# Kernel optimization log

Hardware: AMD Instinct MI355X
Metric: run time of the kernel (lower is better)

## Reference

```python
import jax, jax.numpy as jnp
import numpy as np

B, T = 32, 512
D_TOK, D_OH, D_DEP = 256, 32, 32
D = D_TOK + D_OH + D_DEP  # tree_input_size = 320
H = 64                    # tree_lstm_h_size
P, L, ROOT = 16384, 16, 8 # pairs, path length, root position on path
N = P * L
E = P * (L - 1)
NUM_LEVELS = 9            # max level = max(ROOT, L-1-ROOT) = 8 -> levels 0..8


def _structure():
    # Each subgraph is a shortest path in the dependency tree; edges on both
    # sides point toward the topological root (position ROOT).
    pos = np.arange(L)
    par = np.where(pos < ROOT, pos + 1, np.where(pos > ROOT, pos - 1, pos))
    base = (np.arange(P) * L)[:, None]
    parent_of = (base + par[None, :]).reshape(-1).astype(np.int32)
    nodes = (base + pos[None, :]).reshape(-1).astype(np.int32)
    is_root = np.tile(pos == ROOT, P)
    child = nodes[~is_root]
    parent = parent_of[~is_root]
    level_up = np.tile(np.where(pos <= ROOT, pos, L - 1 - pos), P).astype(np.int32)
    level_down = np.tile(np.abs(pos - ROOT), P).astype(np.int32)
    root_idx = (np.arange(P) * L + ROOT).astype(np.int32)
    start_idx = (np.arange(P) * L).astype(np.int32)
    end_idx = (np.arange(P) * L + (L - 1)).astype(np.int32)
    return child, parent, parent_of, level_up, level_down, root_idx, start_idx, end_idx


def setup_inputs() -> dict:
    key = jax.random.key(0)
    ks = jax.random.split(key, 24)
    sc = 0.02
    ch, pa, po, lu, ld, ri, si, ei = _structure()
    inp = {
        'token_embs': jax.random.normal(ks[0], (B, T, D_TOK), jnp.float32),
        'one_hot_embs': (jax.random.uniform(ks[1], (B, T, D_OH)) < 0.1).astype(jnp.float32),
        'dep_embs': jax.random.normal(ks[2], (B, T, D_DEP), jnp.float32),
        'node_b_idx': jax.random.randint(ks[3], (N,), 0, B, jnp.int32),
        'node_t_idx': jax.random.randint(ks[4], (N,), 0, T, jnp.int32),
        'child': jnp.asarray(ch), 'parent': jnp.asarray(pa),
        'parent_of': jnp.asarray(po),
        'level_up': jnp.asarray(lu), 'level_down': jnp.asarray(ld),
        'root_idx': jnp.asarray(ri), 'start_idx': jnp.asarray(si), 'end_idx': jnp.asarray(ei),
        # child-sum Tree-LSTM params, upward (bottom-up) direction
        'W_iou_up': jax.random.normal(ks[5], (D, 3 * H)) * sc,
        'U_iou_up': jax.random.normal(ks[6], (H, 3 * H)) * sc,
        'b_iou_up': jnp.zeros((3 * H,), jnp.float32),
        'W_f_up': jax.random.normal(ks[7], (D, H)) * sc,
        'U_f_up': jax.random.normal(ks[8], (H, H)) * sc,
        'b_f_up': jnp.zeros((H,), jnp.float32),
        # downward (top-down) direction
        'W_iou_dn': jax.random.normal(ks[9], (D, 3 * H)) * sc,
        'U_iou_dn': jax.random.normal(ks[10], (H, 3 * H)) * sc,
        'b_iou_dn': jnp.zeros((3 * H,), jnp.float32),
        'W_f_dn': jax.random.normal(ks[11], (D, H)) * sc,
        'U_f_dn': jax.random.normal(ks[12], (H, H)) * sc,
        'b_f_dn': jnp.zeros((H,), jnp.float32),
    }
    return inp


def _tree_lstm(x, child, parent, level, x_iou, x_f, U_iou, U_f):
    # Level-synchronous child-sum Tree-LSTM toward parents (bottom-up).
    n = x.shape[0]
    h0 = jnp.zeros((n, H), x.dtype)
    c0 = jnp.zeros((n, H), x.dtype)

    def step(carry, t):
        h, c = carry
        hs = jax.ops.segment_sum(h[child], parent, num_segments=n)          # sum child h
        f = jax.nn.sigmoid(x_f[parent] + h[child] @ U_f)                    # per-edge forget
        fc = jax.ops.segment_sum(f * c[child], parent, num_segments=n)
        i, o, u = jnp.split(x_iou + hs @ U_iou, 3, axis=-1)
        c_new = jax.nn.sigmoid(i) * jnp.tanh(u) + fc
        h_new = jax.nn.sigmoid(o) * jnp.tanh(c_new)
        m = (level == t)[:, None]
        return (jnp.where(m, h_new, h), jnp.where(m, c_new, c)), None

    (h, c), _ = jax.lax.scan(step, (h0, c0), jnp.arange(NUM_LEVELS))
    return h


def _tree_lstm_down(x, parent_of, level_down, x_iou, x_f, U_iou, U_f):
    # Top-down pass: each node has exactly one predecessor (its parent).
    n = x.shape[0]
    not_root = (level_down != 0).astype(x.dtype)[:, None]
    h0 = jnp.zeros((n, H), x.dtype)
    c0 = jnp.zeros((n, H), x.dtype)

    def step(carry, t):
        h, c = carry
        hp = h[parent_of] * not_root
        cp = c[parent_of] * not_root
        f = jax.nn.sigmoid(x_f + hp @ U_f)
        i, o, u = jnp.split(x_iou + hp @ U_iou, 3, axis=-1)
        c_new = jax.nn.sigmoid(i) * jnp.tanh(u) + f * cp
        h_new = jax.nn.sigmoid(o) * jnp.tanh(c_new)
        m = (level_down == t)[:, None]
        return (jnp.where(m, h_new, h), jnp.where(m, c_new, c)), None

    (h, c), _ = jax.lax.scan(step, (h0, c0), jnp.arange(NUM_LEVELS))
    return h


def reference(token_embs, one_hot_embs, dep_embs, node_b_idx, node_t_idx,
              child, parent, parent_of, level_up, level_down,
              root_idx, start_idx, end_idx,
              W_iou_up, U_iou_up, b_iou_up, W_f_up, U_f_up, b_f_up,
              W_iou_dn, U_iou_dn, b_iou_dn, W_f_dn, U_f_dn, b_f_dn):
    # node_embs = cat(token, one_hot, dep) gathered at subgraph node ids (_ID)
    full = jnp.concatenate((token_embs, one_hot_embs, dep_embs), axis=-1)  # [B,T,D]
    x = full[node_b_idx, node_t_idx]                                       # [N,D]

    # precompute input projections once
    xi_u = x @ W_iou_up + b_iou_up
    xf_u = x @ W_f_up + b_f_up
    xi_d = x @ W_iou_dn + b_iou_dn
    xf_d = x @ W_f_dn + b_f_dn

    h_up = _tree_lstm(x, child, parent, level_up, xi_u, xf_u, U_iou_up, U_f_up)
    h_dn = _tree_lstm_down(x, parent_of, level_down, xi_d, xf_d, U_iou_dn, U_f_dn)

    # tree_lstm_out.view(-1,2,H): slot 0 = bottom-up, slot 1 = top-down
    tree_pair_embs = jnp.concatenate(
        (h_up[root_idx], h_dn[start_idx], h_dn[end_idx]), axis=-1)          # [P, 3H]
    return tree_pair_embs
```

## Files before the change

kernel.cpp:

```cpp
#include <hip/hip_runtime.h>
#include <hip/hip_fp16.h>


typedef _Float16 f16x8 __attribute__((ext_vector_type(8)));
typedef _Float16 f16x4 __attribute__((ext_vector_type(4)));
typedef _Float16 f16x2 __attribute__((ext_vector_type(2)));
typedef float f32x4 __attribute__((ext_vector_type(4)));

#define NP 16
#define N2K 2.8853900817779268f

__device__ __forceinline__ void async16(const void* g, void* l) {
    __builtin_amdgcn_global_load_lds(
        (const __attribute__((address_space(1))) void*)g,
        (__attribute__((address_space(3))) void*)l, 16, 0, 0);
}
__device__ __forceinline__ void lgkm_barrier() {
    asm volatile("s_waitcnt lgkmcnt(0)\n\ts_barrier" ::: "memory");
}
__device__ __forceinline__ f32x4 exp2v(f32x4 x) {
    f32x4 y;
    y[0] = __builtin_amdgcn_exp2f(x[0]);
    y[1] = __builtin_amdgcn_exp2f(x[1]);
    y[2] = __builtin_amdgcn_exp2f(x[2]);
    y[3] = __builtin_amdgcn_exp2f(x[3]);
    return y;
}
__device__ __forceinline__ f32x4 rcpv(f32x4 x) {
    f32x4 y;
    y[0] = __builtin_amdgcn_rcpf(x[0]);
    y[1] = __builtin_amdgcn_rcpf(x[1]);
    y[2] = __builtin_amdgcn_rcpf(x[2]);
    y[3] = __builtin_amdgcn_rcpf(x[3]);
    return y;
}

__global__ __launch_bounds__(256) void prep_kernel(
    const float* __restrict__ Wi_u, const float* __restrict__ Ui_u,
    const float* __restrict__ bi_u, const float* __restrict__ Wf_u,
    const float* __restrict__ Uf_u, const float* __restrict__ bf_u,
    const float* __restrict__ Wi_d, const float* __restrict__ Ui_d,
    const float* __restrict__ bi_d, const float* __restrict__ Wf_d,
    const float* __restrict__ Uf_d, const float* __restrict__ bf_d,
    _Float16* __restrict__ Bx, _Float16* __restrict__ Upk,
    float* __restrict__ pb)
{
    int idx = blockIdx.x * 256 + threadIdx.x;
    if (idx < 512) {
        int d = idx >> 8, c = idx & 255, u = c >> 2, g = c & 3;
        const float* bio = d ? bi_d : bi_u;
        const float* bf  = d ? bf_d : bf_u;
        float s = (g == 2) ? -N2K : -0.5f * N2K;
        pb[idx] = s * ((g < 3) ? bio[g * 64 + u] : bf[u]);
    }
    if (idx < 163840) {
        int d = idx / 81920, r1 = idx % 81920;
        int c = r1 / 320, k = r1 % 320, u = c >> 2, g = c & 3;
        const float* Wio = d ? Wi_d : Wi_u;
        const float* Wf  = d ? Wf_d : Wf_u;
        float s = (g == 2) ? -N2K : -0.5f * N2K;
        Bx[idx] = (_Float16)(s * ((g < 3) ? Wio[k * 192 + g * 64 + u]
                                          : Wf[k * 64 + u]));
    } else {
        int j = idx - 163840;
        int d = j >> 14, r2 = j & 16383;
        int g = r2 >> 12, u = (r2 >> 6) & 63, k = r2 & 63;
        const float* Uio = d ? Ui_d : Ui_u;
        const float* Uf  = d ? Uf_d : Uf_u;
        float s = (g == 2) ? -N2K : -0.5f * N2K;
        Upk[j] = (_Float16)(s * ((g < 3) ? Uio[k * 192 + g * 64 + u]
                                         : Uf[k * 64 + u]));
    }
}

__global__ __launch_bounds__(256, 2) void xp_gemm(
    const float* __restrict__ tok, const float* __restrict__ oh,
    const float* __restrict__ dep,
    const _Float16* __restrict__ Bx, const float* __restrict__ pb,
    _Float16* __restrict__ XP)
{
    __shared__ _Float16 At[32 * 64];
    __shared__ _Float16 Btl[256 * 64];
    const int dir = blockIdx.x & 1, mt = blockIdx.x >> 1;
    const int tid = threadIdx.x, lane = tid & 63, w = tid >> 6;
    const int l15 = lane & 15, qd = lane >> 4;
    const int rsub = lane >> 3, pg = lane & 7;
    const int kg = (pg - rsub) & 7;
    const int koff = kg * 8;
    const int rowbase = mt * 32;
    const _Float16* Bb = Bx + (size_t)dir * 81920 + (w * 64 + rsub) * 320 + koff;

    f32x4 acc[2][4];
    #pragma unroll
    for (int i = 0; i < 2; ++i)
        #pragma unroll
        for (int j = 0; j < 4; ++j) acc[i][j] = (f32x4){0.f, 0.f, 0.f, 0.f};

    #pragma unroll
    for (int kt = 0; kt < 5; ++kt) {
        {
            int row = rowbase + w * 8 + rsub;
            int g = kt * 8 + kg;
            const float* src = (g < 32) ? tok + (size_t)row * 256 + g * 8
                             : (g < 36) ? oh  + (size_t)row * 32 + (g - 32) * 8
                                        : dep + (size_t)row * 32 + (g - 36) * 8;
            float4 f0 = *(const float4*)src;
            float4 f1 = *(const float4*)(src + 4);
            f16x8 v;
            v[0] = (_Float16)f0.x; v[1] = (_Float16)f0.y;
            v[2] = (_Float16)f0.z; v[3] = (_Float16)f0.w;
            v[4] = (_Float16)f1.x; v[5] = (_Float16)f1.y;
            v[6] = (_Float16)f1.z; v[7] = (_Float16)f1.w;
            *(f16x8*)&At[(w * 8 + rsub) * 64 + pg * 8] = v;
        }
        #pragma unroll
        for (int is = 0; is < 8; ++is)
            async16(Bb + (size_t)is * 8 * 320 + kt * 64,
                    &Btl[(w * 64 + is * 8) * 64]);
        __syncthreads();
        #pragma unroll
        for (int s = 0; s < 2; ++s) {
            const int g0 = s * 4 + qd;
            f16x8 af[2];
            #pragma unroll
            for (int i = 0; i < 2; ++i) {
                int R = i * 16 + l15;
                af[i] = *(const f16x8*)&At[R * 64 + ((g0 + R) & 7) * 8];
            }
            #pragma unroll
            for (int j = 0; j < 4; ++j) {
                int C = j * 64 + w * 16 + l15;
                f16x8 bf = *(const f16x8*)&Btl[C * 64 + ((g0 + C) & 7) * 8];
                #pragma unroll
                for (int i = 0; i < 2; ++i)
                    acc[i][j] = __builtin_amdgcn_mfma_f32_16x16x32_f16(
                        af[i], bf, acc[i][j], 0, 0, 0);
            }
        }
        __syncthreads();
    }
    #pragma unroll
    for (int i = 0; i < 2; ++i)
        #pragma unroll
        for (int j = 0; j < 4; ++j) {
            int colp = j * 64 + w * 16 + l15;
            float bias = pb[dir * 256 + colp];
            #pragma unroll
            for (int r = 0; r < 4; ++r) {
                int row = rowbase + i * 16 + qd * 4 + r;
                XP[(size_t)row * 512 + dir * 256 + colp] =
                    (_Float16)(acc[i][j][r] + bias);
            }
        }
}

template<int RPP>
__device__ __forceinline__ void gather_xp(
    const char* __restrict__ XPd, const int (*btl)[NP],
    int p0, int p1, int unit, int qd, f16x4* px)
{
    #pragma unroll
    for (int i = 0; i < RPP; ++i)
        #pragma unroll
        for (int r = 0; r < 4; ++r) {
            int row = i * 16 + qd * 4 + r;
            int pl  = (RPP == 2) ? (row >> 1) : row;
            int pos = (RPP == 2) ? ((row & 1) ? p1 : p0) : p0;
            px[i * 4 + r] = *(const f16x4*)(XPd + btl[pos][pl] + unit * 8);
        }
}

template<int RPP>
__device__ __forceinline__ void side_level(
    const f16x8 (*bfr)[4], const f16x4* px,
    const _Float16 (*hR)[68], const _Float16 (*cR)[68],
    _Float16 (*hW)[68], _Float16 (*cWl)[68],
    f16x2* crR, f16x2* crW, int cregr, int cwEn,
    float* __restrict__ out, int pair0,
    int rs0, int rs1, int oc0, int oc1,
    int unit, int l15, int qd)
{
    f32x4 acc[RPP][4];
    #pragma unroll
    for (int i = 0; i < RPP; ++i)
        #pragma unroll
        for (int r = 0; r < 4; ++r) {
            f16x4 g4 = px[i * 4 + r];
            acc[i][0][r] = (float)g4[0];
            acc[i][1][r] = (float)g4[1];
            acc[i][2][r] = (float)g4[2];
            acc[i][3][r] = (float)g4[3];
        }

    if (rs0 >= 0) {
        __builtin_amdgcn_s_setprio(1);
        #pragma unroll
        for (int s = 0; s < 2; ++s)
            #pragma unroll
            for (int i = 0; i < RPP; ++i) {
                int R = i * 16 + l15;
                int arow = (RPP == 2) ? ((R & ~1) | ((R & 1) ? rs1 : rs0))
                                      : (R * 2 + rs0);
                f16x8 af = *(const f16x8*)&hR[arow][s * 32 + qd * 8];
                #pragma unroll
                for (int g = 0; g < 4; ++g)
                    acc[i][g] = __builtin_amdgcn_mfma_f32_16x16x32_f16(
                        af, bfr[s][g], acc[i][g], 0, 0, 0);
            }
        __builtin_amdgcn_s_setprio(0);
    }

    const int nocin = (rs0 < 0 && rs1 < 0);
    #pragma unroll
    for (int i = 0; i < RPP; ++i) {
        f32x4 EA = exp2v(acc[i][0]);
        f32x4 EO = exp2v(acc[i][1]);
        f32x4 EB = exp2v(acc[i][2]);
        f32x4 PQ = (1.f + EA) * (1.f + EB);
        f32x4 CN;
        if (nocin) {
            CN = (1.f - EB) * rcpv(PQ);
        } else {
            f32x4 CIN;
            #pragma unroll
            for (int r = 0; r < 4; ++r) {
                int row = i * 16 + qd * 4 + r;
                int pl   = (RPP == 2) ? (row >> 1) : row;
                int slot = (RPP == 2) ? (row & 1) : 0;
                int rs = slot ? rs1 : rs0;
                if (RPP == 2 && cregr)
                    CIN[r] = (float)crR[i * 2 + (r >> 1)][rs];
                else
                    CIN[r] = (rs >= 0) ? (float)cR[pl * 2 + rs][unit] : 0.f;
            }
            f32x4 EC = exp2v(acc[i][3]);
            f32x4 PC = 1.f + EC;
            f32x4 NUM = CIN * PQ + (1.f - EB) * PC;
            CN = NUM * rcpv(PQ * PC);
        }
        f32x4 EE = exp2v(-N2K * CN);
        f32x4 H = (1.f - EE) * rcpv((1.f + EE) * (1.f + EO));
        #pragma unroll
        for (int r = 0; r < 4; ++r) {
            int row = i * 16 + qd * 4 + r;
            int pl   = (RPP == 2) ? (row >> 1) : row;
            int slot = (RPP == 2) ? (row & 1) : 0;
            int oc = slot ? oc1 : oc0;
            if (oc >= 0) {
                out[(size_t)(pair0 + pl) * 192 + oc + unit] = H[r];
            } else {
                hW[pl * 2 + slot][unit] = (_Float16)H[r];
                if (cwEn) cWl[pl * 2 + slot][unit] = (_Float16)CN[r];
                if (RPP == 2) crW[i * 2 + (r >> 1)][r & 1] = (_Float16)CN[r];
            }
        }
    }
}

__device__ __forceinline__ void root_level(
    const f16x8 (*bfr)[4], const f16x4* px,
    const _Float16 (*hR0)[68], const _Float16 (*cR0)[68],
    const _Float16 (*hR1)[68], const _Float16 (*cR1)[68],
    float* __restrict__ out, int pair0, int unit, int l15, int qd)
{
    f32x4 aio[3], aF7, aF9;
    #pragma unroll
    for (int r = 0; r < 4; ++r) {
        f16x4 g4 = px[r];
        aio[0][r] = (float)g4[0];
        aio[1][r] = (float)g4[1];
        aio[2][r] = (float)g4[2];
        aF7[r] = (float)g4[3];
        aF9[r] = (float)g4[3];
    }
    __builtin_amdgcn_s_setprio(1);
    #pragma unroll
    for (int s = 0; s < 2; ++s) {
        f16x8 v7 = *(const f16x8*)&hR0[l15 * 2 + 0][s * 32 + qd * 8];
        f16x8 v9 = *(const f16x8*)&hR1[l15 * 2 + 1][s * 32 + qd * 8];
        f16x8 vs = v7 + v9;
        aio[0] = __builtin_amdgcn_mfma_f32_16x16x32_f16(vs, bfr[s][0], aio[0], 0, 0, 0);
        aio[1] = __builtin_amdgcn_mfma_f32_16x16x32_f16(vs, bfr[s][1], aio[1], 0, 0, 0);
        aio[2] = __builtin_amdgcn_mfma_f32_16x16x32_f16(vs, bfr[s][2], aio[2], 0, 0, 0);
        aF7 = __builtin_amdgcn_mfma_f32_16x16x32_f16(v7, bfr[s][3], aF7, 0, 0, 0);
        aF9 = __builtin_amdgcn_mfma_f32_16x16x32_f16(v9, bfr[s][3], aF9, 0, 0, 0);
    }
    __builtin_amdgcn_s_setprio(0);
    f32x4 C7, C9;
    #pragma unroll
    for (int r = 0; r < 4; ++r) {
        int pl = qd * 4 + r;
        C7[r] = (float)cR0[pl * 2 + 0][unit];
        C9[r] = (float)cR1[pl * 2 + 1][unit];
    }
    f32x4 EA = exp2v(aio[0]);
    f32x4 EO = exp2v(aio[1]);
    f32x4 EB = exp2v(aio[2]);
    f32x4 E7 = exp2v(aF7);
    f32x4 E9 = exp2v(aF9);
    f32x4 PQ  = (1.f + EA) * (1.f + EB);
    f32x4 S7  = 1.f + E7, S9 = 1.f + E9;
    f32x4 S79 = S7 * S9;
    f32x4 NUM = PQ * (C7 * S9 + C9 * S7) + (1.f - EB) * S79;
    f32x4 CN  = NUM * rcpv(PQ * S79);
    f32x4 EE  = exp2v(-N2K * CN);
    f32x4 H   = (1.f - EE) * rcpv((1.f + EE) * (1.f + EO));
    #pragma unroll
    for (int r = 0; r < 4; ++r) {
        int pl = qd * 4 + r;
        out[(size_t)(pair0 + pl) * 192 + unit] = H[r];
    }
}

__global__ __launch_bounds__(256, 2) void tree_kernel(
    const int* __restrict__ nb, const int* __restrict__ nt,
    const _Float16* __restrict__ XP, const _Float16* __restrict__ Upk,
    float* __restrict__ out)
{
    __shared__ _Float16 hS[2][2][NP * 2][68];
    __shared__ _Float16 cS[2][2][NP * 2][68];
    __shared__ int btl[16][NP];

    const int tid = threadIdx.x, lane = tid & 63, w = tid >> 6;
    const int l15 = lane & 15, qd = lane >> 4;
    const int unit = w * 16 + l15;
    const int pair0 = blockIdx.x * NP;

    {
        int pos = tid >> 4, pl = tid & 15;
        int node = (pair0 + pl) * 16 + pos;
        btl[pos][pl] = (nb[node] * 512 + nt[node]) * 1024;
    }

    f16x8 bU[2][4], bD[2][4];
    #pragma unroll
    for (int s = 0; s < 2; ++s)
        #pragma unroll
        for (int g = 0; g < 4; ++g) {
            bU[s][g] = *(const f16x8*)(Upk + (g * 64 + unit) * 64 + s * 32 + qd * 8);
            bD[s][g] = *(const f16x8*)(Upk + 16384 + (g * 64 + unit) * 64 + s * 32 + qd * 8);
        }

    __syncthreads();

    const char* XPu = (const char*)XP;
    const char* XPdn = XPu + 512;

    f16x2 creg[2][2][4] = {};

    f16x4 pxu[3][8], pxd[8];
    gather_xp<2>(XPu, btl, 0, 15, unit, qd, pxu[0]);
    gather_xp<2>(XPu, btl, 1, 14, unit, qd, pxu[1]);

    #pragma unroll
    for (int t = 0; t < 9; ++t) {
        const int pt = t & 1, pw = pt ^ 1;
        const int cur = t % 3, nx2 = (t + 2) % 3;
        if (t == 0)      gather_xp<1>(XPdn, btl, 8, 8, unit, qd, pxd);
        else if (t == 8) gather_xp<1>(XPdn, btl, 0, 0, unit, qd, pxd);
        else             gather_xp<2>(XPdn, btl, 8 - t, 8 + t, unit, qd, pxd);
        if (t < 5)       gather_xp<2>(XPu, btl, t + 2, 13 - t, unit, qd, pxu[nx2]);
        else if (t == 5) gather_xp<1>(XPu, btl, 7, 7, unit, qd, pxu[nx2]);
        else if (t == 6) gather_xp<1>(XPu, btl, 8, 8, unit, qd, pxu[nx2]);

        if (t < 7)
            side_level<2>(bU, pxu[cur], hS[pt][0], cS[pt][0],
                          hS[pw][0], cS[pw][0],
                          creg[pt][0], creg[pw][0],
                          (t >= 1) ? 1 : 0, (t == 6) ? 1 : 0,
                          out, pair0,
                          t ? 0 : -1, t ? 1 : -1, -1, -1, unit, l15, qd);
        else if (t == 7)
            side_level<1>(bU, pxu[cur], hS[pt][0], cS[pt][0],
                          hS[pw][0], cS[pw][0],
                          creg[pt][0], creg[pw][0], 0, 1,
                          out, pair0,
                          0, 0, -1, -1, unit, l15, qd);
        else
            root_level(bU, pxu[cur], hS[0][0], cS[0][0], hS[1][0], cS[1][0],
                       out, pair0, unit, l15, qd);

        if (t == 0)
            side_level<1>(bD, pxd, hS[pt][1], cS[pt][1],
                          hS[pw][1], cS[pw][1],
                          creg[pt][1], creg[pw][1], 0, 1,
                          out, pair0,
                          -1, -1, -1, -1, unit, l15, qd);
        else if (t == 8)
            side_level<1>(bD, pxd, hS[pt][1], cS[pt][1],
                          hS[pw][1], cS[pw][1],
                          creg[pt][1], creg[pw][1], 0, 0,
                          out, pair0,
                          0, 0, 64, 64, unit, l15, qd);
        else
            side_level<2>(bD, pxd, hS[pt][1], cS[pt][1],
                          hS[pw][1], cS[pw][1],
                          creg[pt][1], creg[pw][1],
                          (t >= 2) ? 1 : 0, (t == 7) ? 1 : 0,
                          out, pair0,
                          0, (t == 1) ? 0 : 1, -1, (t == 7) ? 128 : -1,
                          unit, l15, qd);

        lgkm_barrier();
    }
}

extern "C" void kernel_launch(void* const* d_in, const int* in_sizes, int n_in,
                              void* d_out, int out_size, void* d_ws, size_t ws_size,
                              hipStream_t stream)
{
    const float* tok  = (const float*)d_in[0];
    const float* ohp  = (const float*)d_in[1];
    const float* dep  = (const float*)d_in[2];
    const int*   nb   = (const int*)d_in[3];
    const int*   nt   = (const int*)d_in[4];
    const float* Wi_u = (const float*)d_in[13];
    const float* Ui_u = (const float*)d_in[14];
    const float* bi_u = (const float*)d_in[15];
    const float* Wf_u = (const float*)d_in[16];
    const float* Uf_u = (const float*)d_in[17];
    const float* bf_u = (const float*)d_in[18];
    const float* Wi_d = (const float*)d_in[19];
    const float* Ui_d = (const float*)d_in[20];
    const float* bi_d = (const float*)d_in[21];
    const float* Wf_d = (const float*)d_in[22];
    const float* Uf_d = (const float*)d_in[23];
    const float* bf_d = (const float*)d_in[24];

    char* ws = (char*)d_ws;
    _Float16* Bx  = (_Float16*)(ws);
    _Float16* Upk = (_Float16*)(ws + 0x50000);
    float*    pb  = (float*)   (ws + 0x60000);
    _Float16* XP  = (_Float16*)(ws + (12u << 20));
    float* out = (float*)d_out;

    prep_kernel<<<768, 256, 0, stream>>>(Wi_u, Ui_u, bi_u, Wf_u, Uf_u, bf_u,
                                         Wi_d, Ui_d, bi_d, Wf_d, Uf_d, bf_d,
                                         Bx, Upk, pb);
    xp_gemm<<<1024, 256, 0, stream>>>(tok, ohp, dep, Bx, pb, XP);
    tree_kernel<<<1024, 256, 0, stream>>>(nb, nt, XP, Upk, out);

    (void)in_sizes; (void)n_in; (void)out_size; (void)ws_size;
}
```

Baseline: 185.5 us.

## Halve pairs per block in tree kernel to raise occupancy

Each tree_kernel block now handles 8 pairs instead of 16, doubling the grid to 2048 blocks and raising launch bounds to 5 blocks per CU. Per-level work shrinks from two 16-row MFMA tiles to one, with rows duplicated or masked in single-sided levels. The upward gather prefetch depth drops from two levels to one, and the s_setprio hints are removed. This cuts register and LDS pressure to hide latency through more resident waves, but loses deeper prefetch and wastes half the MFMA rows on single-position levels.

```diff
diff --git a/kernel.cpp b/kernel.cpp
--- a/kernel.cpp
+++ b/kernel.cpp
@@ -7,7 +7,7 @@
 typedef _Float16 f16x2 __attribute__((ext_vector_type(2)));
 typedef float f32x4 __attribute__((ext_vector_type(4)));
 
-#define NP 16
+#define NP 8
 #define N2K 2.8853900817779268f
 
 __device__ __forceinline__ void async16(const void* g, void* l) {
@@ -154,23 +154,21 @@
         }
 }
 
-template<int RPP>
+template<int TWO>
 __device__ __forceinline__ void gather_xp(
     const char* __restrict__ XPd, const int (*btl)[NP],
     int p0, int p1, int unit, int qd, f16x4* px)
 {
     #pragma unroll
-    for (int i = 0; i < RPP; ++i)
-        #pragma unroll
-        for (int r = 0; r < 4; ++r) {
-            int row = i * 16 + qd * 4 + r;
-            int pl  = (RPP == 2) ? (row >> 1) : row;
-            int pos = (RPP == 2) ? ((row & 1) ? p1 : p0) : p0;
-            px[i * 4 + r] = *(const f16x4*)(XPd + btl[pos][pl] + unit * 8);
-        }
-}
-
-template<int RPP>
+    for (int r = 0; r < 4; ++r) {
+        int row = qd * 4 + r;
+        int pl  = TWO ? (row >> 1) : (row & 7);
+        int pos = TWO ? ((row & 1) ? p1 : p0) : p0;
+        px[r] = *(const f16x4*)(XPd + btl[pos][pl] + unit * 8);
+    }
+}
+
+template<int TWO>
 __device__ __forceinline__ void side_level(
     const f16x8 (*bfr)[4], const f16x4* px,
     const _Float16 (*hR)[68], const _Float16 (*cR)[68],
@@ -180,78 +178,71 @@
     int rs0, int rs1, int oc0, int oc1,
     int unit, int l15, int qd)
 {
-    f32x4 acc[RPP][4];
-    #pragma unroll
-    for (int i = 0; i < RPP; ++i)
+    f32x4 acc[4];
+    #pragma unroll
+    for (int r = 0; r < 4; ++r) {
+        f16x4 g4 = px[r];
+        acc[0][r] = (float)g4[0];
+        acc[1][r] = (float)g4[1];
+        acc[2][r] = (float)g4[2];
+        acc[3][r] = (float)g4[3];
+    }
+
+    if (rs0 >= 0) {
+        #pragma unroll
+        for (int s = 0; s < 2; ++s) {
+            int R = l15;
+            int arow = TWO ? ((R & ~1) | ((R & 1) ? rs1 : rs0))
+                           : ((R & 7) * 2 + rs0);
+            f16x8 af = *(const f16x8*)&hR[arow][s * 32 + qd * 8];
+            #pragma unroll
+            for (int g = 0; g < 4; ++g)
+                acc[g] = __builtin_amdgcn_mfma_f32_16x16x32_f16(
+                    af, bfr[s][g], acc[g], 0, 0, 0);
+        }
+    }
+
+    f32x4 EA = exp2v(acc[0]);
+    f32x4 EO = exp2v(acc[1]);
+    f32x4 EB = exp2v(acc[2]);
+    f32x4 PQ = (1.f + EA) * (1.f + EB);
+    f32x4 CN;
+    if (rs0 < 0) {
+        CN = (1.f - EB) * rcpv(PQ);
+    } else {
+        f32x4 CIN;
         #pragma unroll
         for (int r = 0; r < 4; ++r) {
-            f16x4 g4 = px[i * 4 + r];
-            acc[i][0][r] = (float)g4[0];
-            acc[i][1][r] = (float)g4[1];
-            acc[i][2][r] = (float)g4[2];
-            acc[i][3][r] = (float)g4[3];
-        }
-
-    if (rs0 >= 0) {
-        __builtin_amdgcn_s_setprio(1);
-        #pragma unroll
-        for (int s = 0; s < 2; ++s)
-            #pragma unroll
-            for (int i = 0; i < RPP; ++i) {
-                int R = i * 16 + l15;
-                int arow = (RPP == 2) ? ((R & ~1) | ((R & 1) ? rs1 : rs0))
-                                      : (R * 2 + rs0);
-                f16x8 af = *(const f16x8*)&hR[arow][s * 32 + qd * 8];
-                #pragma unroll
-                for (int g = 0; g < 4; ++g)
-                    acc[i][g] = __builtin_amdgcn_mfma_f32_16x16x32_f16(
-                        af, bfr[s][g], acc[i][g], 0, 0, 0);
+            int row = qd * 4 + r;
+            if (TWO) {
+                int rs = (r & 1) ? rs1 : rs0;
+                CIN[r] = cregr ? (float)crR[r >> 1][rs]
+                               : (float)cR[(row >> 1) * 2 + rs][unit];
+            } else {
+                CIN[r] = (float)cR[(row & 7) * 2 + rs0][unit];
             }
-        __builtin_amdgcn_s_setprio(0);
-    }
-
-    const int nocin = (rs0 < 0 && rs1 < 0);
-    #pragma unroll
-    for (int i = 0; i < RPP; ++i) {
-        f32x4 EA = exp2v(acc[i][0]);
-        f32x4 EO = exp2v(acc[i][1]);
-        f32x4 EB = exp2v(acc[i][2]);
-        f32x4 PQ = (1.f + EA) * (1.f + EB);
-        f32x4 CN;
-        if (nocin) {
-            CN = (1.f - EB) * rcpv(PQ);
-        } else {
-            f32x4 CIN;
-            #pragma unroll
-            for (int r = 0; r < 4; ++r) {
-                int row = i * 16 + qd * 4 + r;
-                int pl   = (RPP == 2) ? (row >> 1) : row;
-                int slot = (RPP == 2) ? (row & 1) : 0;
-                int rs = slot ? rs1 : rs0;
-                if (RPP == 2 && cregr)
-                    CIN[r] = (float)crR[i * 2 + (r >> 1)][rs];
-                else
-                    CIN[r] = (rs >= 0) ? (float)cR[pl * 2 + rs][unit] : 0.f;
-            }
-            f32x4 EC = exp2v(acc[i][3]);
-            f32x4 PC = 1.f + EC;
-            f32x4 NUM = CIN * PQ + (1.f - EB) * PC;
-            CN = NUM * rcpv(PQ * PC);
-        }
-        f32x4 EE = exp2v(-N2K * CN);
-        f32x4 H = (1.f - EE) * rcpv((1.f + EE) * (1.f + EO));
+        }
+        f32x4 EC = exp2v(acc[3]);
+        f32x4 PC = 1.f + EC;
+        f32x4 NUM = CIN * PQ + (1.f - EB) * PC;
+        CN = NUM * rcpv(PQ * PC);
+    }
+    f32x4 EE = exp2v(-N2K * CN);
+    f32x4 H = (1.f - EE) * rcpv((1.f + EE) * (1.f + EO));
+
+    if (TWO || qd < 2) {
         #pragma unroll
         for (int r = 0; r < 4; ++r) {
-            int row = i * 16 + qd * 4 + r;
-            int pl   = (RPP == 2) ? (row >> 1) : row;
-            int slot = (RPP == 2) ? (row & 1) : 0;
+            int row = qd * 4 + r;
+            int pl   = TWO ? (row >> 1) : row;
+            int slot = TWO ? (row & 1) : 0;
             int oc = slot ? oc1 : oc0;
             if (oc >= 0) {
                 out[(size_t)(pair0 + pl) * 192 + oc + unit] = H[r];
             } else {
                 hW[pl * 2 + slot][unit] = (_Float16)H[r];
                 if (cwEn) cWl[pl * 2 + slot][unit] = (_Float16)CN[r];
-                if (RPP == 2) crW[i * 2 + (r >> 1)][r & 1] = (_Float16)CN[r];
+                if (TWO)  crW[r >> 1][r & 1] = (_Float16)CN[r];
             }
         }
     }
@@ -273,11 +264,10 @@
         aF7[r] = (float)g4[3];
         aF9[r] = (float)g4[3];
     }
-    __builtin_amdgcn_s_setprio(1);
     #pragma unroll
     for (int s = 0; s < 2; ++s) {
-        f16x8 v7 = *(const f16x8*)&hR0[l15 * 2 + 0][s * 32 + qd * 8];
-        f16x8 v9 = *(const f16x8*)&hR1[l15 * 2 + 1][s * 32 + qd * 8];
+        f16x8 v7 = *(const f16x8*)&hR0[(l15 & 7) * 2 + 0][s * 32 + qd * 8];
+        f16x8 v9 = *(const f16x8*)&hR1[(l15 & 7) * 2 + 1][s * 32 + qd * 8];
         f16x8 vs = v7 + v9;
         aio[0] = __builtin_amdgcn_mfma_f32_16x16x32_f16(vs, bfr[s][0], aio[0], 0, 0, 0);
         aio[1] = __builtin_amdgcn_mfma_f32_16x16x32_f16(vs, bfr[s][1], aio[1], 0, 0, 0);
@@ -285,13 +275,12 @@
         aF7 = __builtin_amdgcn_mfma_f32_16x16x32_f16(v7, bfr[s][3], aF7, 0, 0, 0);
         aF9 = __builtin_amdgcn_mfma_f32_16x16x32_f16(v9, bfr[s][3], aF9, 0, 0, 0);
     }
-    __builtin_amdgcn_s_setprio(0);
     f32x4 C7, C9;
     #pragma unroll
     for (int r = 0; r < 4; ++r) {
-        int pl = qd * 4 + r;
-        C7[r] = (float)cR0[pl * 2 + 0][unit];
-        C9[r] = (float)cR1[pl * 2 + 1][unit];
+        int plc = (qd * 4 + r) & 7;
+        C7[r] = (float)cR0[plc * 2 + 0][unit];
+        C9[r] = (float)cR1[plc * 2 + 1][unit];
     }
     f32x4 EA = exp2v(aio[0]);
     f32x4 EO = exp2v(aio[1]);
@@ -305,14 +294,16 @@
     f32x4 CN  = NUM * rcpv(PQ * S79);
     f32x4 EE  = exp2v(-N2K * CN);
     f32x4 H   = (1.f - EE) * rcpv((1.f + EE) * (1.f + EO));
-    #pragma unroll
-    for (int r = 0; r < 4; ++r) {
-        int pl = qd * 4 + r;
-        out[(size_t)(pair0 + pl) * 192 + unit] = H[r];
-    }
-}
-
-__global__ __launch_bounds__(256, 2) void tree_kernel(
+    if (qd < 2) {
+        #pragma unroll
+        for (int r = 0; r < 4; ++r) {
+            int pl = qd * 4 + r;
+            out[(size_t)(pair0 + pl) * 192 + unit] = H[r];
+        }
+    }
+}
+
+__global__ __launch_bounds__(256, 5) void tree_kernel(
     const int* __restrict__ nb, const int* __restrict__ nt,
     const _Float16* __restrict__ XP, const _Float16* __restrict__ Upk,
     float* __restrict__ out)
@@ -326,8 +317,8 @@
     const int unit = w * 16 + l15;
     const int pair0 = blockIdx.x * NP;
 
-    {
-        int pos = tid >> 4, pl = tid & 15;
+    if (tid < 128) {
+        int pos = tid >> 3, pl = tid & 7;
         int node = (pair0 + pl) * 16 + pos;
         btl[pos][pl] = (nb[node] * 512 + nt[node]) * 1024;
     }
@@ -346,54 +337,52 @@
     const char* XPu = (const char*)XP;
     const char* XPdn = XPu + 512;
 
-    f16x2 creg[2][2][4] = {};
-
-    f16x4 pxu[3][8], pxd[8];
-    gather_xp<2>(XPu, btl, 0, 15, unit, qd, pxu[0]);
-    gather_xp<2>(XPu, btl, 1, 14, unit, qd, pxu[1]);
+    f16x2 creg[2][2][2] = {};
+
+    f16x4 pxu[2][4], pxd[4];
+    gather_xp<1>(XPu, btl, 0, 15, unit, qd, pxu[0]);
 
     #pragma unroll
     for (int t = 0; t < 9; ++t) {
         const int pt = t & 1, pw = pt ^ 1;
-        const int cur = t % 3, nx2 = (t + 2) % 3;
-        if (t == 0)      gather_xp<1>(XPdn, btl, 8, 8, unit, qd, pxd);
-        else if (t == 8) gather_xp<1>(XPdn, btl, 0, 0, unit, qd, pxd);
-        else             gather_xp<2>(XPdn, btl, 8 - t, 8 + t, unit, qd, pxd);
-        if (t < 5)       gather_xp<2>(XPu, btl, t + 2, 13 - t, unit, qd, pxu[nx2]);
-        else if (t == 5) gather_xp<1>(XPu, btl, 7, 7, unit, qd, pxu[nx2]);
-        else if (t == 6) gather_xp<1>(XPu, btl, 8, 8, unit, qd, pxu[nx2]);
+        if (t == 0)      gather_xp<0>(XPdn, btl, 8, 8, unit, qd, pxd);
+        else if (t == 8) gather_xp<0>(XPdn, btl, 0, 0, unit, qd, pxd);
+        else             gather_xp<1>(XPdn, btl, 8 - t, 8 + t, unit, qd, pxd);
+        if (t < 6)       gather_xp<1>(XPu, btl, t + 1, 14 - t, unit, qd, pxu[pw]);
+        else if (t == 6) gather_xp<0>(XPu, btl, 7, 7, unit, qd, pxu[pw]);
+        else if (t == 7) gather_xp<0>(XPu, btl, 8, 8, unit, qd, pxu[pw]);
 
         if (t < 7)
-            side_level<2>(bU, pxu[cur], hS[pt][0], cS[pt][0],
+            side_level<1>(bU, pxu[pt], hS[pt][0], cS[pt][0],
                           hS[pw][0], cS[pw][0],
                           creg[pt][0], creg[pw][0],
                           (t >= 1) ? 1 : 0, (t == 6) ? 1 : 0,
                           out, pair0,
                           t ? 0 : -1, t ? 1 : -1, -1, -1, unit, l15, qd);
         else if (t == 7)
-            side_level<1>(bU, pxu[cur], hS[pt][0], cS[pt][0],
+            side_level<0>(bU, pxu[pt], hS[pt][0], cS[pt][0],
                           hS[pw][0], cS[pw][0],
                           creg[pt][0], creg[pw][0], 0, 1,
                           out, pair0,
                           0, 0, -1, -1, unit, l15, qd);
         else
-            root_level(bU, pxu[cur], hS[0][0], cS[0][0], hS[1][0], cS[1][0],
+            root_level(bU, pxu[pt], hS[0][0], cS[0][0], hS[1][0], cS[1][0],
                        out, pair0, unit, l15, qd);
 
         if (t == 0)
-            side_level<1>(bD, pxd, hS[pt][1], cS[pt][1],
+            side_level<0>(bD, pxd, hS[pt][1], cS[pt][1],
                           hS[pw][1], cS[pw][1],
                           creg[pt][1], creg[pw][1], 0, 1,
                           out, pair0,
                           -1, -1, -1, -1, unit, l15, qd);
         else if (t == 8)
-            side_level<1>(bD, pxd, hS[pt][1], cS[pt][1],
+            side_level<0>(bD, pxd, hS[pt][1], cS[pt][1],
                           hS[pw][1], cS[pw][1],
                           creg[pt][1], creg[pw][1], 0, 0,
                           out, pair0,
                           0, 0, 64, 64, unit, l15, qd);
         else
-            side_level<2>(bD, pxd, hS[pt][1], cS[pt][1],
+            side_level<1>(bD, pxd, hS[pt][1], cS[pt][1],
                           hS[pw][1], cS[pw][1],
                           creg[pt][1], creg[pw][1],
                           (t >= 2) ? 1 : 0, (t == 7) ? 1 : 0,
@@ -438,7 +427,7 @@
                                          Wi_d, Ui_d, bi_d, Wf_d, Uf_d, bf_d,
                                          Bx, Upk, pb);
     xp_gemm<<<1024, 256, 0, stream>>>(tok, ohp, dep, Bx, pb, XP);
-    tree_kernel<<<1024, 256, 0, stream>>>(nb, nt, XP, Upk, out);
+    tree_kernel<<<2048, 256, 0, stream>>>(nb, nt, XP, Upk, out);
 
     (void)in_sizes; (void)n_in; (void)out_size; (void)ws_size;
 }
```

After: 295.1 us. +59.1%, slower.
